# Kernel tuning notes

Measured on AMD Instinct MI355X. Metric: run time of the kernel, lower is better.

The kernel has to match this reference:

```python
import jax, jax.numpy as jnp
import numpy as np

FEATS = 768
HEAD = 12
HD = FEATS // HEAD


def setup_inputs() -> dict:
    key = jax.random.key(0)
    ks = jax.random.split(key, 10)
    b, n, f = 8, 1024, FEATS
    s = 1.0 / np.sqrt(f)
    return {
        "x": jax.random.normal(ks[0], (b, n, f), dtype=jnp.float32),
        "bias": jnp.zeros((), dtype=jnp.float32),
        "Wq": jax.random.normal(ks[1], (f, f), dtype=jnp.float32) * s,
        "bq": jnp.zeros((f,), dtype=jnp.float32),
        "Wk": jax.random.normal(ks[2], (f, f), dtype=jnp.float32) * s,
        "bk": jnp.zeros((f,), dtype=jnp.float32),
        "Wv": jax.random.normal(ks[3], (f, f), dtype=jnp.float32) * s,
        "bv": jnp.zeros((f,), dtype=jnp.float32),
        "Wo": jax.random.normal(ks[4], (f, f), dtype=jnp.float32) * s,
        "bo": jnp.zeros((f,), dtype=jnp.float32),
    }


def reference(x, bias, Wq, bq, Wk, bk, Wv, bv, Wo, bo):
    b, n, f = x.shape
    sqrt_d = jnp.sqrt(jnp.asarray(f, dtype=x.dtype))  # scale uses full feats, per source

    def split_heads(t):  # (b,n,f) -> (b,h,n,hd)
        return t.reshape(b, n, HEAD, HD).transpose(0, 2, 1, 3)

    q = split_heads(x @ Wq.T + bq)
    k = split_heads(x @ Wk.T + bk)
    v = split_heads(x @ Wv.T + bv)

    # sigmoid attention: no row-wise normalization
    score = jax.nn.sigmoid(jnp.einsum('bhif,bhjf->bhij', q, k) / sqrt_d + bias)
    attn = jnp.einsum('bhij,bhjf->bihf', score, v)  # (b,n,h,hd)
    o = attn.reshape(b, n, f) @ Wo.T + bo  # dropout p=0.0 -> identity
    return o
```

## Files before the change

### kernel.cpp

```cpp
#include <hip/hip_runtime.h>

#define FEATS 768
#define NHEAD 12
#define HD    64
#define SEQ   1024
#define NB    8
#define MROWS (NB*SEQ)
#define NQK   (2*FEATS)
#define QKVN  (3*FEATS)
#define QSC   0.0520616136f

typedef __attribute__((ext_vector_type(8))) __bf16          bf16x8;
typedef __attribute__((ext_vector_type(4))) __bf16          bf16x4;
typedef __attribute__((ext_vector_type(4))) unsigned short  us4;
typedef __attribute__((ext_vector_type(4))) float           f32x4;

__device__ __forceinline__ unsigned short f2bf(float f) {
  union { float f; unsigned u; } v; v.f = f;
  return (unsigned short)((v.u + 0x7fffu + ((v.u >> 16) & 1u)) >> 16);
}

__device__ __forceinline__ void gload_lds16(const void* g, void* l) {
  __builtin_amdgcn_global_load_lds(
      (const __attribute__((address_space(1))) void*)g,
      (__attribute__((address_space(3))) void*)l, 16, 0, 0);
}

__global__ void cast_all(const float* __restrict__ x,
                         const float* __restrict__ Wq, const float* __restrict__ Wk,
                         const float* __restrict__ Wv, const float* __restrict__ Wo,
                         const float* __restrict__ bq, const float* __restrict__ bk,
                         const float* __restrict__ bv,
                         unsigned short* __restrict__ Xbf,
                         unsigned short* __restrict__ Wcat,
                         unsigned short* __restrict__ Wobf,
                         float* __restrict__ bcat) {
  int blk = blockIdx.x;
  if (blk < 6144) {
    int i = blk * 256 + threadIdx.x;
    f32x4 v = ((const f32x4*)x)[i];
    us4 o;
    o[0] = f2bf(v[0]); o[1] = f2bf(v[1]); o[2] = f2bf(v[2]); o[3] = f2bf(v[3]);
    ((us4*)Xbf)[i] = o;
  } else if (blk < 8448) {
    int bb = blk - 6144;
    int mtx = bb / 576;
    int i = (bb % 576) * 256 + threadIdx.x;
    const float* src = (mtx == 0) ? Wq : (mtx == 1) ? Wk : (mtx == 2) ? Wv : Wo;
    f32x4 v = ((const f32x4*)src)[i];
    us4 o;
    o[0] = f2bf(v[0]); o[1] = f2bf(v[1]); o[2] = f2bf(v[2]); o[3] = f2bf(v[3]);
    if (mtx < 3) ((us4*)Wcat)[mtx * 147456 + i] = o;
    else         ((us4*)Wobf)[i] = o;
  } else {
    int i = (blk - 8448) * 256 + threadIdx.x;
    if (i < QKVN)
      bcat[i] = (i < FEATS) ? bq[i] : (i < 2*FEATS ? bk[i-FEATS] : bv[i-2*FEATS]);
  }
}

#define FOFF(row) ((row)*64 + (((g) ^ (((row) >> 1) & 3)) << 4))

__global__ __launch_bounds__(256, 3) void gemm1_bt(
    const unsigned short* __restrict__ A,
    const unsigned short* __restrict__ B,
    const float* __restrict__ bias,
    unsigned short* __restrict__ QKo,
    unsigned short* __restrict__ VTo)
{
  __shared__ __align__(16) char Al[2 * 8192];
  __shared__ __align__(16) char Bl[3 * 12288];

  const int tid  = threadIdx.x;
  const int lane = tid & 63;
  const int w    = tid >> 6;
  const int l15  = lane & 15;
  const int g    = lane >> 4;
  const int wm   = (w >> 1) * 64;
  const int wn   = (w & 1) * 96;

  const int id  = blockIdx.x;
  const int xcd = id & 7;
  const int j   = id >> 3;
  const int mi  = xcd * 8 + (j & 7);
  const int ni  = j >> 3;
  const int mbase = mi * 128;
  const int nbase = ni * 192;

  const int trow  = tid >> 2;
  const int sslot = ((tid & 3) ^ ((tid >> 3) & 3)) * 8;
  const unsigned short* Ag = A + (size_t)(mbase + trow) * 768 + sslot;
  const unsigned short* Bg = B + (size_t)(nbase + trow) * 768 + sslot;

  auto STAGE_A = [&](int buf, int t) {
    const unsigned short* sa = Ag + t * 32;
    char* da = Al + buf * 8192 + tid * 16;
    gload_lds16(sa,            da);
    gload_lds16(sa + 64*768,   da + 4096);
  };
  auto STAGE_B = [&](int buf, int t) {
    const unsigned short* sb = Bg + t * 32;
    char* db = Bl + buf * 12288 + tid * 16;
    gload_lds16(sb,            db);
    gload_lds16(sb + 64*768,   db + 4096);
    gload_lds16(sb + 128*768,  db + 8192);
  };

  f32x4 acc[4][6] = {};

  STAGE_A(0, 0);
  STAGE_B(0, 0);
  STAGE_B(1, 1);
  asm volatile("s_waitcnt vmcnt(3)" ::: "memory");
  __builtin_amdgcn_s_barrier();

  for (int t = 0; t < 24; t++) {
    if (t < 23) STAGE_A((t + 1) & 1, t + 1);
    if (t < 22) STAGE_B((t + 2) % 3, t + 2);

    const char* Ab = Al + (t & 1) * 8192;
    const char* Bb = Bl + (t % 3) * 12288;
    bf16x8 af[4];
#pragma unroll
    for (int mf = 0; mf < 4; mf++) {
      const int row = wm + mf*16 + l15;
      af[mf] = *(const bf16x8*)(Ab + FOFF(row));
    }
    __builtin_amdgcn_s_setprio(1);
#pragma unroll
    for (int nf = 0; nf < 6; nf++) {
      const int row = wn + nf*16 + l15;
      bf16x8 bfv = *(const bf16x8*)(Bb + FOFF(row));
#pragma unroll
      for (int mf = 0; mf < 4; mf++)
        acc[mf][nf] = __builtin_amdgcn_mfma_f32_16x16x32_bf16(af[mf], bfv, acc[mf][nf], 0, 0, 0);
    }
    __builtin_amdgcn_s_setprio(0);

    if (t < 23) {
      if (t < 22) asm volatile("s_waitcnt vmcnt(3)" ::: "memory");
      else        asm volatile("s_waitcnt vmcnt(0)" ::: "memory");
      __builtin_amdgcn_s_barrier();
    }
  }

  const bool isQK = (ni < 8);
  const float osc = (ni < 4) ? QSC : 1.0f;
#pragma unroll
  for (int mf = 0; mf < 4; mf++)
#pragma unroll
    for (int nf = 0; nf < 6; nf++) {
      const int col  = nbase + wn + nf*16 + l15;
      const float bb = bias[col];
      const int row0 = mbase + wm + mf*16 + g*4;
      if (isQK) {
#pragma unroll
        for (int r = 0; r < 4; r++)
          QKo[(size_t)(row0 + r)*NQK + col] = f2bf((acc[mf][nf][r] + bb) * osc);
      } else {
        const int c  = col - NQK;
        const int hh = c >> 6, dd = c & 63;
        const int bI = row0 >> 10, n0 = row0 & 1023;
        const int rl  = n0 & 63;
        const int cp  = ((rl >> 5) << 5) | (((rl >> 2) & 3) << 3) | (((rl >> 4) & 1) << 2);
        const int n0p = (n0 & ~63) | cp;
        us4 o;
#pragma unroll
        for (int r = 0; r < 4; r++) o[r] = f2bf(acc[mf][nf][r] + bb);
        *(us4*)(VTo + ((size_t)((bI*NHEAD + hh)*HD + dd))*SEQ + n0p) = o;
      }
    }
}

__global__ __launch_bounds__(256, 4) void gemm2_bt(
    const unsigned short* __restrict__ A,
    const unsigned short* __restrict__ B,
    const float* __restrict__ bias,
    float* __restrict__ C)
{
  __shared__ __align__(16) char Al[2 * 4096];
  __shared__ __align__(16) char Bl[3 * 8192];

  const int tid  = threadIdx.x;
  const int lane = tid & 63;
  const int w    = tid >> 6;
  const int l15  = lane & 15;
  const int g    = lane >> 4;
  const int wm   = (w >> 1) * 32;
  const int wn   = (w & 1) * 64;

  const int id  = blockIdx.x;
  const int xcd = id & 7;
  const int j   = id >> 3;
  const int mi  = xcd * 16 + (j & 15);
  const int ni  = j >> 4;
  const int mbase = mi * 64;
  const int nbase = ni * 128;

  const int trow  = tid >> 2;
  const int sslot = ((tid & 3) ^ ((tid >> 3) & 3)) * 8;
  const unsigned short* Ag = A + (size_t)(mbase + trow) * 768 + sslot;
  const unsigned short* Bg = B + (size_t)(nbase + trow) * 768 + sslot;

  auto STAGE_A = [&](int buf, int t) {
    char* da = Al + buf * 4096 + tid * 16;
    gload_lds16(Ag + t * 32, da);
  };
  auto STAGE_B = [&](int buf, int t) {
    const unsigned short* sb = Bg + t * 32;
    char* db = Bl + buf * 8192 + tid * 16;
    gload_lds16(sb,           db);
    gload_lds16(sb + 64*768,  db + 4096);
  };

  f32x4 acc[2][4] = {};

  STAGE_A(0, 0);
  STAGE_B(0, 0);
  STAGE_B(1, 1);
  asm volatile("s_waitcnt vmcnt(2)" ::: "memory");
  __builtin_amdgcn_s_barrier();

  for (int t = 0; t < 24; t++) {
    if (t < 23) STAGE_A((t + 1) & 1, t + 1);
    if (t < 22) STAGE_B((t + 2) % 3, t + 2);

    const char* Ab = Al + (t & 1) * 4096;
    const char* Bb = Bl + (t % 3) * 8192;
    bf16x8 af[2], bfv[4];
#pragma unroll
    for (int mf = 0; mf < 2; mf++) {
      const int row = wm + mf*16 + l15;
      af[mf] = *(const bf16x8*)(Ab + FOFF(row));
    }
#pragma unroll
    for (int nf = 0; nf < 4; nf++) {
      const int row = wn + nf*16 + l15;
      bfv[nf] = *(const bf16x8*)(Bb + FOFF(row));
    }
    __builtin_amdgcn_s_setprio(1);
#pragma unroll
    for (int mf = 0; mf < 2; mf++)
#pragma unroll
      for (int nf = 0; nf < 4; nf++)
        acc[mf][nf] = __builtin_amdgcn_mfma_f32_16x16x32_bf16(af[mf], bfv[nf], acc[mf][nf], 0, 0, 0);
    __builtin_amdgcn_s_setprio(0);

    if (t < 23) {
      if (t < 22) asm volatile("s_waitcnt vmcnt(2)" ::: "memory");
      else        asm volatile("s_waitcnt vmcnt(0)" ::: "memory");
      __builtin_amdgcn_s_barrier();
    }
  }

#pragma unroll
  for (int mf = 0; mf < 2; mf++)
#pragma unroll
    for (int nf = 0; nf < 4; nf++) {
      const int col  = nbase + wn + nf*16 + l15;
      const float bb = bias[col];
      const int row0 = mbase + wm + mf*16 + g*4;
#pragma unroll
      for (int r = 0; r < 4; r++)
        C[(size_t)(row0 + r)*FEATS + col] = acc[mf][nf][r] + bb;
    }
}
#undef FOFF

__global__ __launch_bounds__(256, 3) void attn_kernel(
    const unsigned short* __restrict__ QK,
    const unsigned short* __restrict__ VT,
    const float* __restrict__ biasp,
    unsigned short* __restrict__ AO)
{
  __shared__ __align__(16) char Kl[2][8192];
  __shared__ __align__(16) char Vl[2][8192];

  const int tid  = threadIdx.x;
  const int lane = tid & 63;
  const int w    = tid >> 6;
  const int l15  = lane & 15;
  const int g    = lane >> 4;

  const int id  = blockIdx.x;
  const int r8  = id & 7;
  const int m   = id >> 3;
  const int bh  = r8 * 12 + (m >> 3);
  const int qx  = m & 7;
  const int b   = bh / NHEAD;
  const int h   = bh % NHEAD;
  const int rowB  = b * SEQ;
  const int qbase = rowB + qx * 128;

  const float Kb = __builtin_amdgcn_exp2f(-biasp[0] * 1.4426950408889634f);

  bf16x8 qf[2][2];
  {
    const unsigned short* qp = QK + (size_t)(qbase + w*32 + l15) * NQK + h*HD + g*8;
    qf[0][0] = *(const bf16x8*)(qp);
    qf[0][1] = *(const bf16x8*)(qp + 32);
    qf[1][0] = *(const bf16x8*)(qp + 16*NQK);
    qf[1][1] = *(const bf16x8*)(qp + 16*NQK + 32);
  }

  const int trow = tid >> 3;
  const int colb = ((tid & 7) * 16) ^ ((trow & 7) << 4);
  const char* Ksrc = (const char*)QK +
      ((size_t)(rowB + trow) * NQK + FEATS + h*HD) * 2 + colb;
  const char* Vsrc = (const char*)VT +
      ((size_t)(bh*HD + trow)) * (SEQ*2) + colb;

  auto STAGE_K = [&](int p, int t) {
    char* kw = Kl[p] + tid*16;
    gload_lds16(Ksrc + (size_t)t * 64 * (NQK*2),              kw);
    gload_lds16(Ksrc + (size_t)t * 64 * (NQK*2) + 32*(NQK*2), kw + 4096);
  };
  auto STAGE_V = [&](int p, int t) {
    char* vw = Vl[p] + tid*16;
    gload_lds16(Vsrc + t * 128,              vw);
    gload_lds16(Vsrc + t * 128 + 32*(SEQ*2), vw + 4096);
  };

  f32x4 o_acc[4][2] = {};
  f32x4 sE[2][4], sO[2][4];

  auto SIGPV = [&](f32x4 (&sP)[2][4], const char* Vp) {
    bf16x8 paq[2][2];
#pragma unroll
    for (int qm = 0; qm < 2; qm++) {
      float sg[4][4];
#pragma unroll
      for (int nf = 0; nf < 4; nf++)
#pragma unroll
        for (int rr = 0; rr < 4; rr++) {
          const float e = __builtin_amdgcn_exp2f(-sP[qm][nf][rr]);
          sg[nf][rr] = __builtin_amdgcn_rcpf(__builtin_fmaf(Kb, e, 1.0f));
        }
#pragma unroll
      for (int js = 0; js < 2; js++) {
        bf16x8 pa;
#pragma unroll
        for (int jj = 0; jj < 4; jj++) {
          pa[jj]     = (__bf16)sg[2*js][jj];
          pa[jj + 4] = (__bf16)sg[2*js + 1][jj];
        }
        paq[qm][js] = pa;
      }
    }
#pragma unroll
    for (int js = 0; js < 2; js++) {
      bf16x8 vf[4];
#pragma unroll
      for (int df = 0; df < 4; df++) {
        const int row = df*16 + l15;
        const int by  = (row*128 + js*64 + g*16) ^ ((row & 7) << 4);
        vf[df] = *(const bf16x8*)(Vp + by);
      }
      __builtin_amdgcn_s_setprio(1);
#pragma unroll
      for (int df = 0; df < 4; df++)
#pragma unroll
        for (int qm = 0; qm < 2; qm++)
          o_acc[df][qm] = __builtin_amdgcn_mfma_f32_16x16x32_bf16(vf[df], paq[qm][js], o_acc[df][qm], 0, 0, 0);
      __builtin_amdgcn_s_setprio(0);
    }
  };

  auto BODY = [&](int t, f32x4 (&sC)[2][4], f32x4 (&sP)[2][4], bool stK, bool doPrev) {
    if (stK) STAGE_K((t + 1) & 1, t + 1);
    STAGE_V(t & 1, t);

    const char* Kp = Kl[t & 1];
#pragma unroll
    for (int qm = 0; qm < 2; qm++)
#pragma unroll
      for (int nf = 0; nf < 4; nf++)
        sC[qm][nf] = (f32x4){0.f, 0.f, 0.f, 0.f};
    __builtin_amdgcn_s_setprio(1);
#pragma unroll
    for (int nf = 0; nf < 4; nf++)
#pragma unroll
      for (int ks = 0; ks < 2; ks++) {
        const int row = nf*16 + l15;
        const int by  = (row*128 + ks*64 + g*16) ^ ((row & 7) << 4);
        bf16x8 kf = *(const bf16x8*)(Kp + by);
        sC[0][nf] = __builtin_amdgcn_mfma_f32_16x16x32_bf16(kf, qf[0][ks], sC[0][nf], 0, 0, 0);
        sC[1][nf] = __builtin_amdgcn_mfma_f32_16x16x32_bf16(kf, qf[1][ks], sC[1][nf], 0, 0, 0);
      }
    __builtin_amdgcn_s_setprio(0);

    if (doPrev) SIGPV(sP, Vl[(t - 1) & 1]);

    __syncthreads();
  };

  STAGE_K(0, 0);
  __syncthreads();

  BODY(0, sE, sO, true, false);
#pragma unroll 1
  for (int t = 1; t < 15; t += 2) {
    BODY(t,     sO, sE, true, true);
    BODY(t + 1, sE, sO, true, true);
  }
  BODY(15, sO, sE, false, true);
  SIGPV(sO, Vl[1]);

  unsigned short* aop = AO + (size_t)(qbase + w*32) * FEATS + h*HD;
#pragma unroll
  for (int df = 0; df < 4; df++)
#pragma unroll
    for (int qm = 0; qm < 2; qm++) {
      const int q  = qm*16 + l15;
      const int d0 = df*16 + g*4;
      bf16x4 o;
#pragma unroll
      for (int rr = 0; rr < 4; rr++) o[rr] = (__bf16)o_acc[df][qm][rr];
      *(bf16x4*)(aop + (size_t)q * FEATS + d0) = o;
    }
}

extern "C" void kernel_launch(void* const* d_in, const int* in_sizes, int n_in,
                              void* d_out, int out_size, void* d_ws, size_t ws_size,
                              hipStream_t stream) {
  const float* x    = (const float*)d_in[0];
  const float* bias = (const float*)d_in[1];
  const float* Wq   = (const float*)d_in[2];
  const float* bq   = (const float*)d_in[3];
  const float* Wk   = (const float*)d_in[4];
  const float* bk   = (const float*)d_in[5];
  const float* Wv   = (const float*)d_in[6];
  const float* bv   = (const float*)d_in[7];
  const float* Wo   = (const float*)d_in[8];
  const float* bo   = (const float*)d_in[9];
  float* out = (float*)d_out;

  char* ws = (char*)d_ws;
  unsigned short* Xbf  = (unsigned short*)(ws + 0);
  unsigned short* Wcat = (unsigned short*)(ws + 12582912);
  unsigned short* Wobf = (unsigned short*)(ws + 16121856);
  float*          bcat = (float*)        (ws + 17301504);
  unsigned short* QKb  = (unsigned short*)(ws + 17310720);
  unsigned short* VTb  = (unsigned short*)(ws + 42476544);
  unsigned short* AO   = Xbf;

  cast_all<<<8457, 256, 0, stream>>>(x, Wq, Wk, Wv, Wo, bq, bk, bv,
                                     Xbf, Wcat, Wobf, bcat);

  gemm1_bt<<<768, 256, 0, stream>>>(Xbf, Wcat, bcat, QKb, VTb);

  attn_kernel<<<768, 256, 0, stream>>>(QKb, VTb, bias, AO);

  gemm2_bt<<<768, 256, 0, stream>>>(AO, Wobf, bo, out);
}
```

Measured before the change: 105.1 us.

## Enlarge QKV GEMM tiles to 256x288 with 512 threads and split-K double buffering

```diff
diff --git a/kernel.cpp b/kernel.cpp
--- a/kernel.cpp
+++ b/kernel.cpp
@@ -61,15 +61,15 @@
 
 #define FOFF(row) ((row)*64 + (((g) ^ (((row) >> 1) & 3)) << 4))
 
-__global__ __launch_bounds__(256, 3) void gemm1_bt(
+__global__ __launch_bounds__(512, 2) void gemm1_bt(
     const unsigned short* __restrict__ A,
     const unsigned short* __restrict__ B,
     const float* __restrict__ bias,
     unsigned short* __restrict__ QKo,
     unsigned short* __restrict__ VTo)
 {
-  __shared__ __align__(16) char Al[2 * 8192];
-  __shared__ __align__(16) char Bl[3 * 12288];
+  __shared__ __align__(16) char Al[2 * 2 * 16384];
+  __shared__ __align__(16) char Bl[2 * 2 * 18432];
 
   const int tid  = threadIdx.x;
   const int lane = tid & 63;
@@ -77,83 +77,95 @@
   const int l15  = lane & 15;
   const int g    = lane >> 4;
   const int wm   = (w >> 1) * 64;
-  const int wn   = (w & 1) * 96;
+  const int wn   = (w & 1) * 144;
 
   const int id  = blockIdx.x;
   const int xcd = id & 7;
   const int j   = id >> 3;
-  const int mi  = xcd * 8 + (j & 7);
-  const int ni  = j >> 3;
-  const int mbase = mi * 128;
-  const int nbase = ni * 192;
+  const int mi  = xcd * 4 + (j >> 3);
+  const int ni  = j & 7;
+  const int mbase = mi * 256;
+  const int nbase = ni * 288;
 
   const int trow  = tid >> 2;
   const int sslot = ((tid & 3) ^ ((tid >> 3) & 3)) * 8;
-  const unsigned short* Ag = A + (size_t)(mbase + trow) * 768 + sslot;
-  const unsigned short* Bg = B + (size_t)(nbase + trow) * 768 + sslot;
-
-  auto STAGE_A = [&](int buf, int t) {
-    const unsigned short* sa = Ag + t * 32;
-    char* da = Al + buf * 8192 + tid * 16;
-    gload_lds16(sa,            da);
-    gload_lds16(sa + 64*768,   da + 4096);
-  };
-  auto STAGE_B = [&](int buf, int t) {
-    const unsigned short* sb = Bg + t * 32;
-    char* db = Bl + buf * 12288 + tid * 16;
-    gload_lds16(sb,            db);
-    gload_lds16(sb + 64*768,   db + 4096);
-    gload_lds16(sb + 128*768,  db + 8192);
-  };
-
-  f32x4 acc[4][6] = {};
-
-  STAGE_A(0, 0);
-  STAGE_B(0, 0);
-  STAGE_B(1, 1);
-  asm volatile("s_waitcnt vmcnt(3)" ::: "memory");
+  const unsigned short* Ag  = A + (size_t)(mbase + trow) * 768 + sslot;
+  const unsigned short* Bg  = B + (size_t)(nbase + trow) * 768 + sslot;
+  const unsigned short* Bg2 = B + (size_t)(nbase + 256 + ((tid & 127) >> 2)) * 768 + sslot;
+
+  auto STAGE_A = [&](int buf, int t, int kh) {
+    const unsigned short* sa = Ag + t*64 + kh*32;
+    char* da = Al + (buf*2 + kh) * 16384 + tid * 16;
+    gload_lds16(sa,             da);
+    gload_lds16(sa + 128*768,   da + 8192);
+  };
+  auto STAGE_B = [&](int buf, int t, int kh) {
+    const unsigned short* sb = Bg + t*64 + kh*32;
+    char* db = Bl + (buf*2 + kh) * 18432 + tid * 16;
+    gload_lds16(sb,             db);
+    gload_lds16(sb + 128*768,   db + 8192);
+    gload_lds16(Bg2 + t*64 + kh*32,
+                Bl + (buf*2 + kh) * 18432 + 16384 + (tid & 127) * 16);
+  };
+
+  f32x4 acc[4][9] = {};
+
+  STAGE_A(0, 0, 0); STAGE_B(0, 0, 0);
+  STAGE_A(0, 0, 1); STAGE_B(0, 0, 1);
+  STAGE_A(1, 1, 0); STAGE_B(1, 1, 0);
+  asm volatile("s_waitcnt vmcnt(10)" ::: "memory");
   __builtin_amdgcn_s_barrier();
 
-  for (int t = 0; t < 24; t++) {
-    if (t < 23) STAGE_A((t + 1) & 1, t + 1);
-    if (t < 22) STAGE_B((t + 2) % 3, t + 2);
-
-    const char* Ab = Al + (t & 1) * 8192;
-    const char* Bb = Bl + (t % 3) * 12288;
-    bf16x8 af[4];
-#pragma unroll
-    for (int mf = 0; mf < 4; mf++) {
-      const int row = wm + mf*16 + l15;
-      af[mf] = *(const bf16x8*)(Ab + FOFF(row));
-    }
+#pragma unroll 1
+  for (int q = 0; q < 24; q++) {
+    const int t   = q >> 1;
+    const int kh  = q & 1;
+    const int buf = t & 1;
+
+    if (q <= 20) {
+      const int h2  = q + 3;
+      const int t2  = h2 >> 1;
+      const int kh2 = h2 & 1;
+      STAGE_A(t2 & 1, t2, kh2);
+      STAGE_B(t2 & 1, t2, kh2);
+    }
+
+    const char* Ab = Al + (buf*2 + kh) * 16384;
+    const char* Bb = Bl + (buf*2 + kh) * 18432;
+    bf16x8 af[4], bfv[9];
+#pragma unroll
+    for (int mf = 0; mf < 4; mf++)
+      af[mf] = *(const bf16x8*)(Ab + FOFF(wm + mf*16 + l15));
+#pragma unroll
+    for (int nf = 0; nf < 9; nf++)
+      bfv[nf] = *(const bf16x8*)(Bb + FOFF(wn + nf*16 + l15));
+
+    __builtin_amdgcn_s_barrier();
+    asm volatile("s_waitcnt lgkmcnt(0)" ::: "memory");
     __builtin_amdgcn_s_setprio(1);
 #pragma unroll
-    for (int nf = 0; nf < 6; nf++) {
-      const int row = wn + nf*16 + l15;
-      bf16x8 bfv = *(const bf16x8*)(Bb + FOFF(row));
+    for (int nf = 0; nf < 9; nf++)
 #pragma unroll
       for (int mf = 0; mf < 4; mf++)
-        acc[mf][nf] = __builtin_amdgcn_mfma_f32_16x16x32_bf16(af[mf], bfv, acc[mf][nf], 0, 0, 0);
-    }
+        acc[mf][nf] = __builtin_amdgcn_mfma_f32_16x16x32_bf16(af[mf], bfv[nf], acc[mf][nf], 0, 0, 0);
     __builtin_amdgcn_s_setprio(0);
 
-    if (t < 23) {
-      if (t < 22) asm volatile("s_waitcnt vmcnt(3)" ::: "memory");
-      else        asm volatile("s_waitcnt vmcnt(0)" ::: "memory");
-      __builtin_amdgcn_s_barrier();
-    }
+    if (q <= 20)      asm volatile("s_waitcnt vmcnt(10)" ::: "memory");
+    else if (q == 21) asm volatile("s_waitcnt vmcnt(5)"  ::: "memory");
+    else if (q == 22) asm volatile("s_waitcnt vmcnt(0)"  ::: "memory");
+    if (q < 23) __builtin_amdgcn_s_barrier();
   }
 
-  const bool isQK = (ni < 8);
-  const float osc = (ni < 4) ? QSC : 1.0f;
 #pragma unroll
   for (int mf = 0; mf < 4; mf++)
 #pragma unroll
-    for (int nf = 0; nf < 6; nf++) {
-      const int col  = nbase + wn + nf*16 + l15;
+    for (int nf = 0; nf < 9; nf++) {
+      const int c16  = nbase + wn + nf*16;
+      const int col  = c16 + l15;
       const float bb = bias[col];
       const int row0 = mbase + wm + mf*16 + g*4;
-      if (isQK) {
+      if (c16 < NQK) {
+        const float osc = (c16 < FEATS) ? QSC : 1.0f;
 #pragma unroll
         for (int r = 0; r < 4; r++)
           QKo[(size_t)(row0 + r)*NQK + col] = f2bf((acc[mf][nf][r] + bb) * osc);
@@ -447,7 +459,7 @@
   cast_all<<<8457, 256, 0, stream>>>(x, Wq, Wk, Wv, Wo, bq, bk, bv,
                                      Xbf, Wcat, Wobf, bcat);
 
-  gemm1_bt<<<768, 256, 0, stream>>>(Xbf, Wcat, bcat, QKb, VTb);
+  gemm1_bt<<<256, 512, 0, stream>>>(Xbf, Wcat, bcat, QKb, VTb);
 
   attn_kernel<<<768, 256, 0, stream>>>(QKb, VTb, bias, AO);
 
```

Result: slower. 115.9 us (+10.3%).

## Load QKV GEMM A operand directly into registers, bypassing LDS

Applied to the files above, without the earlier changes.

```diff
diff --git a/kernel.cpp b/kernel.cpp
--- a/kernel.cpp
+++ b/kernel.cpp
@@ -68,7 +68,6 @@
     unsigned short* __restrict__ QKo,
     unsigned short* __restrict__ VTo)
 {
-  __shared__ __align__(16) char Al[2 * 8192];
   __shared__ __align__(16) char Bl[3 * 12288];
 
   const int tid  = threadIdx.x;
@@ -89,14 +88,14 @@
 
   const int trow  = tid >> 2;
   const int sslot = ((tid & 3) ^ ((tid >> 3) & 3)) * 8;
-  const unsigned short* Ag = A + (size_t)(mbase + trow) * 768 + sslot;
   const unsigned short* Bg = B + (size_t)(nbase + trow) * 768 + sslot;
 
-  auto STAGE_A = [&](int buf, int t) {
-    const unsigned short* sa = Ag + t * 32;
-    char* da = Al + buf * 8192 + tid * 16;
-    gload_lds16(sa,            da);
-    gload_lds16(sa + 64*768,   da + 4096);
+  const unsigned short* Arow = A + (size_t)(mbase + wm + l15) * 768 + g * 8;
+
+  auto LOAD_A = [&](bf16x8 (&dst)[4], int t) {
+#pragma unroll
+    for (int mf = 0; mf < 4; mf++)
+      dst[mf] = *(const bf16x8*)(Arow + (size_t)mf * 16 * 768 + t * 32);
   };
   auto STAGE_B = [&](int buf, int t) {
     const unsigned short* sb = Bg + t * 32;
@@ -107,38 +106,43 @@
   };
 
   f32x4 acc[4][6] = {};
-
-  STAGE_A(0, 0);
+  bf16x8 afE[4], afO[4];
+
+  auto COMPUTE = [&](bf16x8 (&af)[4], int t) {
+    const char* Bb = Bl + (t % 3) * 12288;
+    __builtin_amdgcn_s_setprio(1);
+#pragma unroll
+    for (int nf = 0; nf < 6; nf++) {
+      const int row = wn + nf*16 + l15;
+      bf16x8 bfv = *(const bf16x8*)(Bb + FOFF(row));
+#pragma unroll
+      for (int mf = 0; mf < 4; mf++)
+        acc[mf][nf] = __builtin_amdgcn_mfma_f32_16x16x32_bf16(af[mf], bfv, acc[mf][nf], 0, 0, 0);
+    }
+    __builtin_amdgcn_s_setprio(0);
+  };
+
+  LOAD_A(afE, 0);
   STAGE_B(0, 0);
   STAGE_B(1, 1);
   asm volatile("s_waitcnt vmcnt(3)" ::: "memory");
   __builtin_amdgcn_s_barrier();
 
-  for (int t = 0; t < 24; t++) {
-    if (t < 23) STAGE_A((t + 1) & 1, t + 1);
+#pragma unroll 1
+  for (int t = 0; t < 24; t += 2) {
+    LOAD_A(afO, t + 1);
     if (t < 22) STAGE_B((t + 2) % 3, t + 2);
-
-    const char* Ab = Al + (t & 1) * 8192;
-    const char* Bb = Bl + (t % 3) * 12288;
-    bf16x8 af[4];
-#pragma unroll
-    for (int mf = 0; mf < 4; mf++) {
-      const int row = wm + mf*16 + l15;
-      af[mf] = *(const bf16x8*)(Ab + FOFF(row));
-    }
-    __builtin_amdgcn_s_setprio(1);
-#pragma unroll
-    for (int nf = 0; nf < 6; nf++) {
-      const int row = wn + nf*16 + l15;
-      bf16x8 bfv = *(const bf16x8*)(Bb + FOFF(row));
-#pragma unroll
-      for (int mf = 0; mf < 4; mf++)
-        acc[mf][nf] = __builtin_amdgcn_mfma_f32_16x16x32_bf16(af[mf], bfv, acc[mf][nf], 0, 0, 0);
-    }
-    __builtin_amdgcn_s_setprio(0);
-
-    if (t < 23) {
-      if (t < 22) asm volatile("s_waitcnt vmcnt(3)" ::: "memory");
+    COMPUTE(afE, t);
+    if (t < 22) asm volatile("s_waitcnt vmcnt(3)" ::: "memory");
+    else        asm volatile("s_waitcnt vmcnt(0)" ::: "memory");
+    __builtin_amdgcn_s_barrier();
+
+    const int u = t + 1;
+    if (u < 23) LOAD_A(afE, u + 1);
+    if (u < 22) STAGE_B((u + 2) % 3, u + 2);
+    COMPUTE(afO, u);
+    if (u < 23) {
+      if (u < 22) asm volatile("s_waitcnt vmcnt(3)" ::: "memory");
       else        asm volatile("s_waitcnt vmcnt(0)" ::: "memory");
       __builtin_amdgcn_s_barrier();
     }
```

Result: slower. 120.7 us (+14.9%).

## Load K and V fragments directly from global into registers, dropping LDS staging

Applied to the files above, without the earlier changes.

```diff
diff --git a/kernel.cpp b/kernel.cpp
--- a/kernel.cpp
+++ b/kernel.cpp
@@ -273,9 +273,6 @@
     const float* __restrict__ biasp,
     unsigned short* __restrict__ AO)
 {
-  __shared__ __align__(16) char Kl[2][8192];
-  __shared__ __align__(16) char Vl[2][8192];
-
   const int tid  = threadIdx.x;
   const int lane = tid & 63;
   const int w    = tid >> 6;
@@ -303,108 +300,79 @@
     qf[1][1] = *(const bf16x8*)(qp + 16*NQK + 32);
   }
 
-  const int trow = tid >> 3;
-  const int colb = ((tid & 7) * 16) ^ ((trow & 7) << 4);
-  const char* Ksrc = (const char*)QK +
-      ((size_t)(rowB + trow) * NQK + FEATS + h*HD) * 2 + colb;
-  const char* Vsrc = (const char*)VT +
-      ((size_t)(bh*HD + trow)) * (SEQ*2) + colb;
-
-  auto STAGE_K = [&](int p, int t) {
-    char* kw = Kl[p] + tid*16;
-    gload_lds16(Ksrc + (size_t)t * 64 * (NQK*2),              kw);
-    gload_lds16(Ksrc + (size_t)t * 64 * (NQK*2) + 32*(NQK*2), kw + 4096);
-  };
-  auto STAGE_V = [&](int p, int t) {
-    char* vw = Vl[p] + tid*16;
-    gload_lds16(Vsrc + t * 128,              vw);
-    gload_lds16(Vsrc + t * 128 + 32*(SEQ*2), vw + 4096);
-  };
-
+  const unsigned short* Kg = QK + (size_t)(rowB + l15) * NQK + FEATS + h*HD + g*8;
+  const unsigned short* Vg = VT + (size_t)(bh*HD + l15) * SEQ + g*8;
+
+  bf16x8 kf[4][2], vf[4][2];
+  f32x4 s[2][4];
   f32x4 o_acc[4][2] = {};
-  f32x4 sE[2][4], sO[2][4];
-
-  auto SIGPV = [&](f32x4 (&sP)[2][4], const char* Vp) {
+  const f32x4 Zc = {0.f, 0.f, 0.f, 0.f};
+
+  auto LOAD_K = [&](int t) {
+#pragma unroll
+    for (int nf = 0; nf < 4; nf++)
+#pragma unroll
+      for (int ks = 0; ks < 2; ks++)
+        kf[nf][ks] = *(const bf16x8*)(Kg + (size_t)(t*64 + nf*16) * NQK + ks*32);
+  };
+  auto LOAD_V = [&](int t) {
+#pragma unroll
+    for (int df = 0; df < 4; df++)
+#pragma unroll
+      for (int js = 0; js < 2; js++)
+        vf[df][js] = *(const bf16x8*)(Vg + (size_t)(df*16) * SEQ + t*64 + js*32);
+  };
+
+  LOAD_K(0);
+
+#pragma unroll 1
+  for (int t = 0; t < 16; t++) {
+    LOAD_V(t);
+
+    __builtin_amdgcn_s_setprio(1);
+#pragma unroll
+    for (int nf = 0; nf < 4; nf++) {
+      s[0][nf] = __builtin_amdgcn_mfma_f32_16x16x32_bf16(kf[nf][0], qf[0][0], Zc, 0, 0, 0);
+      s[1][nf] = __builtin_amdgcn_mfma_f32_16x16x32_bf16(kf[nf][0], qf[1][0], Zc, 0, 0, 0);
+      s[0][nf] = __builtin_amdgcn_mfma_f32_16x16x32_bf16(kf[nf][1], qf[0][1], s[0][nf], 0, 0, 0);
+      s[1][nf] = __builtin_amdgcn_mfma_f32_16x16x32_bf16(kf[nf][1], qf[1][1], s[1][nf], 0, 0, 0);
+    }
+    __builtin_amdgcn_s_setprio(0);
+
+    if (t < 15) LOAD_K(t + 1);
+
     bf16x8 paq[2][2];
 #pragma unroll
-    for (int qm = 0; qm < 2; qm++) {
-      float sg[4][4];
-#pragma unroll
-      for (int nf = 0; nf < 4; nf++)
+    for (int qm = 0; qm < 2; qm++)
+#pragma unroll
+      for (int js = 0; js < 2; js++) {
+        float s0[4], s1[4];
 #pragma unroll
         for (int rr = 0; rr < 4; rr++) {
-          const float e = __builtin_amdgcn_exp2f(-sP[qm][nf][rr]);
-          sg[nf][rr] = __builtin_amdgcn_rcpf(__builtin_fmaf(Kb, e, 1.0f));
+          const float e0 = __builtin_amdgcn_exp2f(-s[qm][2*js][rr]);
+          s0[rr] = __builtin_amdgcn_rcpf(__builtin_fmaf(Kb, e0, 1.0f));
+          const float e1 = __builtin_amdgcn_exp2f(-s[qm][2*js+1][rr]);
+          s1[rr] = __builtin_amdgcn_rcpf(__builtin_fmaf(Kb, e1, 1.0f));
         }
-#pragma unroll
-      for (int js = 0; js < 2; js++) {
         bf16x8 pa;
 #pragma unroll
         for (int jj = 0; jj < 4; jj++) {
-          pa[jj]     = (__bf16)sg[2*js][jj];
-          pa[jj + 4] = (__bf16)sg[2*js + 1][jj];
+          pa[jj]     = (__bf16)s0[jj];
+          pa[jj + 4] = (__bf16)s1[jj];
         }
         paq[qm][js] = pa;
       }
-    }
-#pragma unroll
-    for (int js = 0; js < 2; js++) {
-      bf16x8 vf[4];
-#pragma unroll
-      for (int df = 0; df < 4; df++) {
-        const int row = df*16 + l15;
-        const int by  = (row*128 + js*64 + g*16) ^ ((row & 7) << 4);
-        vf[df] = *(const bf16x8*)(Vp + by);
-      }
-      __builtin_amdgcn_s_setprio(1);
+
+    __builtin_amdgcn_s_setprio(1);
+#pragma unroll
+    for (int js = 0; js < 2; js++)
 #pragma unroll
       for (int df = 0; df < 4; df++)
 #pragma unroll
         for (int qm = 0; qm < 2; qm++)
-          o_acc[df][qm] = __builtin_amdgcn_mfma_f32_16x16x32_bf16(vf[df], paq[qm][js], o_acc[df][qm], 0, 0, 0);
-      __builtin_amdgcn_s_setprio(0);
-    }
-  };
-
-  auto BODY = [&](int t, f32x4 (&sC)[2][4], f32x4 (&sP)[2][4], bool stK, bool doPrev) {
-    if (stK) STAGE_K((t + 1) & 1, t + 1);
-    STAGE_V(t & 1, t);
-
-    const char* Kp = Kl[t & 1];
-#pragma unroll
-    for (int qm = 0; qm < 2; qm++)
-#pragma unroll
-      for (int nf = 0; nf < 4; nf++)
-        sC[qm][nf] = (f32x4){0.f, 0.f, 0.f, 0.f};
-    __builtin_amdgcn_s_setprio(1);
-#pragma unroll
-    for (int nf = 0; nf < 4; nf++)
-#pragma unroll
-      for (int ks = 0; ks < 2; ks++) {
-        const int row = nf*16 + l15;
-        const int by  = (row*128 + ks*64 + g*16) ^ ((row & 7) << 4);
-        bf16x8 kf = *(const bf16x8*)(Kp + by);
-        sC[0][nf] = __builtin_amdgcn_mfma_f32_16x16x32_bf16(kf, qf[0][ks], sC[0][nf], 0, 0, 0);
-        sC[1][nf] = __builtin_amdgcn_mfma_f32_16x16x32_bf16(kf, qf[1][ks], sC[1][nf], 0, 0, 0);
-      }
+          o_acc[df][qm] = __builtin_amdgcn_mfma_f32_16x16x32_bf16(vf[df][js], paq[qm][js], o_acc[df][qm], 0, 0, 0);
     __builtin_amdgcn_s_setprio(0);
-
-    if (doPrev) SIGPV(sP, Vl[(t - 1) & 1]);
-
-    __syncthreads();
-  };
-
-  STAGE_K(0, 0);
-  __syncthreads();
-
-  BODY(0, sE, sO, true, false);
-#pragma unroll 1
-  for (int t = 1; t < 15; t += 2) {
-    BODY(t,     sO, sE, true, true);
-    BODY(t + 1, sE, sO, true, true);
   }
-  BODY(15, sO, sE, false, true);
-  SIGPV(sO, Vl[1]);
 
   unsigned short* aop = AO + (size_t)(qbase + w*32) * FEATS + h*HD;
 #pragma unroll
```

After: 158.1 us. 50.5% more time.
